# Optimization experiments

Measured on AMD Instinct MI355X. Metric: run time of the kernel, lower is better.

## Reference

```python
import jax, jax.numpy as jnp
import numpy as np

BS, NCH, H, NAGGR, R = 8192, 4, 256, 4, 8  # batch, max_output_degree, h_size, n_aggr, rank


def _xavier(k, shape):
    fan_in = int(np.prod(shape[:-1]))
    fan_out = int(shape[-1])
    s = float(np.sqrt(6.0 / (fan_in + fan_out)))
    return jax.random.uniform(k, shape, jnp.float32, -s, s)


def setup_inputs() -> dict:
    key = jax.random.key(0)
    ks = jax.random.split(key, 6)
    return {
        "neighbour_h": jax.random.normal(ks[0], (BS, NCH, H), jnp.float32),
        "U": _xavier(ks[1], (NCH, NAGGR, H, R)),
        "b": _xavier(ks[2], (NCH, NAGGR, 1, R)),
        "U_out": _xavier(ks[3], (NAGGR, R, H)),
        "b_out": _xavier(ks[4], (NAGGR, 1, H)),
        "T": _xavier(ks[5], (NAGGR,) + (R + 1,) * NCH + (R,)),
    }


def reference(neighbour_h, U, b, U_out, b_out, T):
    bs = neighbour_h.shape[0]
    # per-child projection: matmul([bs,nch,1,1,h], [nch,naggr,h,r]) + b, squeezed -> [bs,nch,naggr,r]
    x = jnp.einsum('bch,cahr->bcar', neighbour_h, U) + b[:, :, 0, :]
    ones = jnp.ones((bs, NAGGR, 1), x.dtype)
    # AugmentedTensor chained contraction (vectorized over the n_aggr loop):
    # first mode: [bs,naggr,r+1] @ [naggr,r+1,(r+1)^(nch-1)*r]
    h0 = jnp.concatenate([x[:, 0], ones], axis=-1)          # [bs,naggr,r+1]
    ris = jnp.einsum('baq,aqx->bax', h0, T.reshape(NAGGR, R + 1, -1))
    for i in range(1, NCH):  # contract remaining modes one by one
        hi = jnp.concatenate([x[:, i], ones], axis=-1)      # [bs,naggr,r+1]
        ris = ris.reshape(bs, NAGGR, R + 1, -1)
        ris = jnp.einsum('baq,baqx->bax', hi, ris)
    # ris: [bs,naggr,r]; output projection + bias -> [bs,naggr,h] -> [bs,naggr*h]
    out = jnp.einsum('bar,arh->bah', ris, U_out) + b_out[:, 0, :]
    return out.reshape(bs, -1)
```

## Files before the change

### kernel.cpp

```cpp
#include <hip/hip_runtime.h>

#define TT_ISTRIDE 672
#define TT_ELEMS (4 * 81 * 672)
#define WS_H   217728
#define WS_RIS 1397376
#define RIS_IHALF_STRIDE 262144

__global__ void t_transpose(const float* __restrict__ T, float* __restrict__ Tt) {
    int idx = blockIdx.x * 256 + threadIdx.x;
    if (idx >= TT_ELEMS) return;
    int col  = idx % 84;
    int t1   = idx / 84;
    int r    = t1 & 7;
    int rest = t1 / 8;
    int jt   = col / 28;
    int kk   = col - jt * 28;
    Tt[idx] = (kk < 27) ? T[rest * 648 + (jt * 27 + kk) * 8 + r] : 0.0f;
}

#define GLL(gsrc, ldst) __builtin_amdgcn_global_load_lds( \
    (const __attribute__((address_space(1))) void*)(gsrc), \
    (__attribute__((address_space(3))) void*)(ldst), 16, 0, 0)

#define KEEP(x) asm volatile("" : "+v"(x))

__global__ __launch_bounds__(512, 4) void k1_phasex(
    const float* __restrict__ nh, const float* __restrict__ U,
    const float* __restrict__ bi, float* __restrict__ h_ws) {
    __shared__ float nh_s[128 * 68];
    __shared__ float u_s[8 * 68];
    const int t  = threadIdx.x;
    const int a  = blockIdx.x >> 6;
    const int b0 = (blockIdx.x & 63) << 7;
    const int b  = t & 127;
    const int rp = t >> 7;

    #pragma unroll 1
    for (int c = 0; c < 4; ++c) {
        float acc0 = 0.f, acc1 = 0.f;
        #pragma unroll 1
        for (int hq = 0; hq < 4; ++hq) {
            __syncthreads();
            #pragma unroll
            for (int k = 0; k < 4; ++k) {
                int idx = t + (k << 9);
                int row = idx >> 4, col = (idx & 15) << 2;
                *(float4*)(nh_s + row * 68 + col) =
                    *(const float4*)(nh + (size_t)(b0 + row) * 1024 + (c << 8) + (hq << 6) + col);
            }
            u_s[(t & 7) * 68 + (t >> 3)] =
                U[(((c << 2) + a) << 11) + (((hq << 6) + (t >> 3)) << 3) + (t & 7)];
            __syncthreads();
            const float* nhp = nh_s + b * 68;
            const float* u0p = u_s + rp * 68;
            const float* u1p = u_s + (rp + 4) * 68;
            #pragma unroll
            for (int hh = 0; hh < 64; hh += 4) {
                float4 v  = *(const float4*)(nhp + hh);
                float4 ua = *(const float4*)(u0p + hh);
                float4 ub = *(const float4*)(u1p + hh);
                acc0 = fmaf(v.x, ua.x, acc0); acc0 = fmaf(v.y, ua.y, acc0);
                acc0 = fmaf(v.z, ua.z, acc0); acc0 = fmaf(v.w, ua.w, acc0);
                acc1 = fmaf(v.x, ub.x, acc1); acc1 = fmaf(v.y, ub.y, acc1);
                acc1 = fmaf(v.z, ub.z, acc1); acc1 = fmaf(v.w, ub.w, acc1);
            }
        }
        acc0 += bi[(((c << 2) + a) << 3) + rp];
        acc1 += bi[(((c << 2) + a) << 3) + rp + 4];
        size_t hb = ((size_t)a * 8192 + b0 + b) * 36 + c * 9;
        h_ws[hb + rp]     = acc0;
        h_ws[hb + rp + 4] = acc1;
        if (rp == 0) h_ws[hb + 8] = 1.0f;
    }
}

__global__ __launch_bounds__(512, 2) void k2_chain(
    const float* __restrict__ Tt, const float* __restrict__ h_ws,
    float* __restrict__ risP) {
    __shared__ float tc[2][9 * 672];
    __shared__ float h_s[36 * 260];

    const int t    = threadIdx.x;
    const int lane = t & 63;
    const int widr = t >> 6;
    const int ihalf = blockIdx.x >> 7;
    const int a     = (blockIdx.x >> 5) & 3;
    const int b0    = (blockIdx.x & 31) << 8;
    const int q0base = ihalf ? 4 : 0;
    const int NC     = ihalf ? 5 : 4;

    const float* Tw = Tt + (size_t)a * 54432 + (size_t)q0base * 6048;

    {
        const float* s = Tw;
        float* d = tc[0];
        GLL(s + 4 * t, d + 4 * t);
        GLL(s + 4 * (512 + t), d + 4 * (512 + t));
        if (t < 488) GLL(s + 4 * (1024 + t), d + 4 * (1024 + t));
    }
    for (int idx = t; idx < 2304; idx += 512) {
        int bb = idx / 9, j = idx % 9;
        float4 v = *(const float4*)(h_ws + ((size_t)a * 8192 + b0 + bb) * 36 + j * 4);
        h_s[(4 * j + 0) * 260 + bb] = v.x;
        h_s[(4 * j + 1) * 260 + bb] = v.y;
        h_s[(4 * j + 2) * 260 + bb] = v.z;
        h_s[(4 * j + 3) * 260 + bb] = v.w;
    }
    __syncthreads();

    float h2v[4][9], h3v[4][9];
    #pragma unroll
    for (int k = 0; k < 4; ++k) {
        #pragma unroll
        for (int q = 0; q < 9; ++q) {
            h2v[k][q] = h_s[(18 + q) * 260 + lane + 64 * k];
            h3v[k][q] = h_s[(27 + q) * 260 + lane + 64 * k];
        }
    }
    #pragma unroll
    for (int k = 0; k < 4; ++k) {
        #pragma unroll
        for (int q = 0; q < 9; ++q) { KEEP(h2v[k][q]); KEEP(h3v[k][q]); }
    }

    float A0 = 0.f, A1 = 0.f, A2 = 0.f, A3 = 0.f;

    #pragma unroll 1
    for (int c = 0; c < NC; ++c) {
        if (c < NC - 1) {
            const float* s = Tw + (size_t)(c + 1) * 6048;
            float* d = tc[(c + 1) & 1];
            GLL(s + 4 * t, d + 4 * t);
            GLL(s + 4 * (512 + t), d + 4 * (512 + t));
            if (t < 488) GLL(s + 4 * (1024 + t), d + 4 * (1024 + t));
            asm volatile("s_waitcnt vmcnt(3)" ::: "memory");
        } else {
            asm volatile("s_waitcnt vmcnt(0)" ::: "memory");
        }
        __builtin_amdgcn_s_barrier();
        asm volatile("" ::: "memory");

        const float* tb = tc[c & 1] + widr * 84;
        float h0c[4];
        #pragma unroll
        for (int k = 0; k < 4; ++k)
            h0c[k] = h_s[(q0base + c) * 260 + lane + 64 * k];

        #pragma unroll 1
        for (int q1 = 0; q1 < 9; ++q1) {
            float h1q[4];
            #pragma unroll
            for (int k = 0; k < 4; ++k)
                h1q[k] = h_s[(9 + q1) * 260 + lane + 64 * k];
            const float* tp = tb + q1 * TT_ISTRIDE;
            float dd[4] = {0.f, 0.f, 0.f, 0.f};
            #pragma unroll
            for (int jt = 0; jt < 3; ++jt) {
                float s[28];
                #pragma unroll
                for (int m = 0; m < 7; ++m)
                    *(float4*)(s + 4 * m) = *(const float4*)(tp + jt * 28 + 4 * m);
                #pragma unroll
                for (int k = 0; k < 4; ++k) {
                    float e0 = 0.f, e1 = 0.f, e2 = 0.f;
                    #pragma unroll
                    for (int m = 0; m < 9; ++m) {
                        e0 = fmaf(s[m],      h3v[k][m], e0);
                        e1 = fmaf(s[9 + m],  h3v[k][m], e1);
                        e2 = fmaf(s[18 + m], h3v[k][m], e2);
                    }
                    dd[k] = fmaf(h2v[k][3 * jt], e0, fmaf(h2v[k][3 * jt + 1], e1,
                            fmaf(h2v[k][3 * jt + 2], e2, dd[k])));
                }
            }
            A0 = fmaf(h0c[0] * h1q[0], dd[0], A0);
            A1 = fmaf(h0c[1] * h1q[1], dd[1], A1);
            A2 = fmaf(h0c[2] * h1q[2], dd[2], A2);
            A3 = fmaf(h0c[3] * h1q[3], dd[3], A3);
        }
        asm volatile("" ::: "memory");
        __builtin_amdgcn_s_barrier();
    }

    size_t rb = (size_t)ihalf * RIS_IHALF_STRIDE + ((size_t)a * 8192 + b0) * 8 + widr;
    risP[rb + (size_t)(lane)       * 8] = A0;
    risP[rb + (size_t)(lane + 64)  * 8] = A1;
    risP[rb + (size_t)(lane + 128) * 8] = A2;
    risP[rb + (size_t)(lane + 192) * 8] = A3;
}

__global__ __launch_bounds__(256, 8) void k3_out(
    const float* __restrict__ risP, const float* __restrict__ Uo,
    const float* __restrict__ bo, float* __restrict__ out) {
    __shared__ float uo_s[8192];
    __shared__ float bo_s[1024];
    __shared__ float ris_s[16 * 32];
    const int t  = threadIdx.x;
    const int b0 = blockIdx.x << 4;
    for (int idx = t; idx < 8192; idx += 256) uo_s[idx] = Uo[idx];
    for (int idx = t; idx < 1024; idx += 256) bo_s[idx] = bo[idx];
    for (int idx = t; idx < 512; idx += 256) {
        int bb = idx >> 5, rem = idx & 31, aa = rem >> 3, rr = rem & 7;
        size_t ro = ((size_t)aa * 8192 + b0 + bb) * 8 + rr;
        ris_s[bb * 32 + rem] = risP[ro] + risP[RIS_IHALF_STRIDE + ro];
    }
    __syncthreads();
    const int a  = t >> 6;
    const int c4 = (t & 63) << 2;
    float4 u[8];
    #pragma unroll
    for (int r = 0; r < 8; ++r)
        u[r] = *(const float4*)(uo_s + (a << 11) + (r << 8) + c4);
    const float4 b4 = *(const float4*)(bo_s + (a << 8) + c4);
    #pragma unroll 4
    for (int bb = 0; bb < 16; ++bb) {
        const float* rp = ris_s + bb * 32 + a * 8;
        float4 v = b4;
        #pragma unroll
        for (int r = 0; r < 8; ++r) {
            float w = rp[r];
            v.x = fmaf(w, u[r].x, v.x); v.y = fmaf(w, u[r].y, v.y);
            v.z = fmaf(w, u[r].z, v.z); v.w = fmaf(w, u[r].w, v.w);
        }
        *(float4*)(out + (size_t)(b0 + bb) * 1024 + (a << 8) + c4) = v;
    }
}

extern "C" void kernel_launch(void* const* d_in, const int* in_sizes, int n_in,
                              void* d_out, int out_size, void* d_ws, size_t ws_size,
                              hipStream_t stream) {
    (void)in_sizes; (void)n_in; (void)out_size; (void)ws_size;
    const float* nh = (const float*)d_in[0];
    const float* U  = (const float*)d_in[1];
    const float* bi = (const float*)d_in[2];
    const float* Uo = (const float*)d_in[3];
    const float* bo = (const float*)d_in[4];
    const float* T  = (const float*)d_in[5];
    float* outp = (float*)d_out;
    float* ws   = (float*)d_ws;

    t_transpose<<<(TT_ELEMS + 255) / 256, 256, 0, stream>>>(T, ws);
    k1_phasex<<<256, 512, 0, stream>>>(nh, U, bi, ws + WS_H);
    k2_chain<<<256, 512, 0, stream>>>(ws, ws + WS_H, ws + WS_RIS);
    k3_out<<<512, 256, 0, stream>>>(ws + WS_RIS, Uo, bo, outp);
}
```

Baseline: 108.7 us.

## Rework projection and chain kernels with transposed workspace and finer i-split

The projection kernel now gives each thread all 8 rank outputs for one child and aggregator. It loads neighbour rows into double-buffered XOR-swizzled LDS via global_load_lds, reads U directly from global memory, and writes h in a transposed [a][36][batch] layout. The chain kernel splits the 81 (q0,q1) pairs into four balanced quarters, doubling the grid to 512 blocks with smaller LDS and higher occupancy. It loads h rows with coalesced float4 reads from the transposed layout. The output kernel sums four partial ris buffers instead of two, adding a little reduction traffic.

New measurement: 113.7 us. 1.05x slower.

```diff
diff --git a/kernel.cpp b/kernel.cpp
--- a/kernel.cpp
+++ b/kernel.cpp
@@ -2,9 +2,9 @@
 
 #define TT_ISTRIDE 672
 #define TT_ELEMS (4 * 81 * 672)
-#define WS_H   217728
-#define WS_RIS 1397376
-#define RIS_IHALF_STRIDE 262144
+#define WS_HT 217728
+#define WS_RIS (217728 + 1179648)
+#define RIS_Q 262144
 
 __global__ void t_transpose(const float* __restrict__ T, float* __restrict__ Tt) {
     int idx = blockIdx.x * 256 + threadIdx.x;
@@ -24,142 +24,169 @@
 
 #define KEEP(x) asm volatile("" : "+v"(x))
 
-__global__ __launch_bounds__(512, 4) void k1_phasex(
+__global__ __launch_bounds__(512, 2) void k1_phasex(
     const float* __restrict__ nh, const float* __restrict__ U,
-    const float* __restrict__ bi, float* __restrict__ h_ws) {
-    __shared__ float nh_s[128 * 68];
-    __shared__ float u_s[8 * 68];
-    const int t  = threadIdx.x;
-    const int a  = blockIdx.x >> 6;
-    const int b0 = (blockIdx.x & 63) << 7;
-    const int b  = t & 127;
-    const int rp = t >> 7;
+    const float* __restrict__ bi, float* __restrict__ h_t) {
+    __shared__ float nh_s[2][8192];
+    const int t   = threadIdx.x;
+    const int bid = blockIdx.x;
+    const int bg  = (bid & 7) * 8 + ((bid >> 3) & 7);
+    const int c   = bid >> 6;
+    const int b0  = bg << 7;
+    const int b   = t & 127;
+    const int a   = t >> 7;
+
+    float acc[8];
+    {
+        const float* bp = bi + (((c << 2) + a) << 3);
+        #pragma unroll
+        for (int r = 0; r < 8; ++r) acc[r] = bp[r];
+    }
+
+    {
+        #pragma unroll
+        for (int rep = 0; rep < 4; ++rep) {
+            int tt = t + (rep << 9);
+            int bl = tt >> 4, sl = tt & 15;
+            const float* s = nh + (size_t)(b0 + bl) * 1024 + (c << 8)
+                           + ((sl ^ (bl & 15)) << 2);
+            GLL(s, &nh_s[0][tt << 2]);
+        }
+    }
 
     #pragma unroll 1
-    for (int c = 0; c < 4; ++c) {
-        float acc0 = 0.f, acc1 = 0.f;
-        #pragma unroll 1
-        for (int hq = 0; hq < 4; ++hq) {
-            __syncthreads();
-            #pragma unroll
-            for (int k = 0; k < 4; ++k) {
-                int idx = t + (k << 9);
-                int row = idx >> 4, col = (idx & 15) << 2;
-                *(float4*)(nh_s + row * 68 + col) =
-                    *(const float4*)(nh + (size_t)(b0 + row) * 1024 + (c << 8) + (hq << 6) + col);
+    for (int w = 0; w < 4; ++w) {
+        if (w < 3) {
+            #pragma unroll
+            for (int rep = 0; rep < 4; ++rep) {
+                int tt = t + (rep << 9);
+                int bl = tt >> 4, sl = tt & 15;
+                const float* s = nh + (size_t)(b0 + bl) * 1024 + (c << 8)
+                               + ((w + 1) << 6) + ((sl ^ (bl & 15)) << 2);
+                GLL(s, &nh_s[(w + 1) & 1][tt << 2]);
             }
-            u_s[(t & 7) * 68 + (t >> 3)] =
-                U[(((c << 2) + a) << 11) + (((hq << 6) + (t >> 3)) << 3) + (t & 7)];
-            __syncthreads();
-            const float* nhp = nh_s + b * 68;
-            const float* u0p = u_s + rp * 68;
-            const float* u1p = u_s + (rp + 4) * 68;
-            #pragma unroll
-            for (int hh = 0; hh < 64; hh += 4) {
-                float4 v  = *(const float4*)(nhp + hh);
-                float4 ua = *(const float4*)(u0p + hh);
-                float4 ub = *(const float4*)(u1p + hh);
-                acc0 = fmaf(v.x, ua.x, acc0); acc0 = fmaf(v.y, ua.y, acc0);
-                acc0 = fmaf(v.z, ua.z, acc0); acc0 = fmaf(v.w, ua.w, acc0);
-                acc1 = fmaf(v.x, ub.x, acc1); acc1 = fmaf(v.y, ub.y, acc1);
-                acc1 = fmaf(v.z, ub.z, acc1); acc1 = fmaf(v.w, ub.w, acc1);
-            }
-        }
-        acc0 += bi[(((c << 2) + a) << 3) + rp];
-        acc1 += bi[(((c << 2) + a) << 3) + rp + 4];
-        size_t hb = ((size_t)a * 8192 + b0 + b) * 36 + c * 9;
-        h_ws[hb + rp]     = acc0;
-        h_ws[hb + rp + 4] = acc1;
-        if (rp == 0) h_ws[hb + 8] = 1.0f;
-    }
-}
-
-__global__ __launch_bounds__(512, 2) void k2_chain(
-    const float* __restrict__ Tt, const float* __restrict__ h_ws,
+            asm volatile("s_waitcnt vmcnt(4)" ::: "memory");
+        } else {
+            asm volatile("s_waitcnt vmcnt(0)" ::: "memory");
+        }
+        __builtin_amdgcn_s_barrier();
+        asm volatile("" ::: "memory");
+
+        const float* Up = U + (((c << 2) + a) << 11) + (w << 9);
+        const float* ap = &nh_s[w & 1][b << 6];
+        #pragma unroll 4
+        for (int k4 = 0; k4 < 16; ++k4) {
+            float4 A = *(const float4*)(ap + ((k4 ^ (b & 15)) << 2));
+            const float4* up = (const float4*)(Up + (k4 << 5));
+            float4 u0 = up[0], u1 = up[1], u2 = up[2], u3 = up[3];
+            float4 u4 = up[4], u5 = up[5], u6 = up[6], u7 = up[7];
+            acc[0]=fmaf(A.x,u0.x,acc[0]); acc[1]=fmaf(A.x,u0.y,acc[1]);
+            acc[2]=fmaf(A.x,u0.z,acc[2]); acc[3]=fmaf(A.x,u0.w,acc[3]);
+            acc[4]=fmaf(A.x,u1.x,acc[4]); acc[5]=fmaf(A.x,u1.y,acc[5]);
+            acc[6]=fmaf(A.x,u1.z,acc[6]); acc[7]=fmaf(A.x,u1.w,acc[7]);
+            acc[0]=fmaf(A.y,u2.x,acc[0]); acc[1]=fmaf(A.y,u2.y,acc[1]);
+            acc[2]=fmaf(A.y,u2.z,acc[2]); acc[3]=fmaf(A.y,u2.w,acc[3]);
+            acc[4]=fmaf(A.y,u3.x,acc[4]); acc[5]=fmaf(A.y,u3.y,acc[5]);
+            acc[6]=fmaf(A.y,u3.z,acc[6]); acc[7]=fmaf(A.y,u3.w,acc[7]);
+            acc[0]=fmaf(A.z,u4.x,acc[0]); acc[1]=fmaf(A.z,u4.y,acc[1]);
+            acc[2]=fmaf(A.z,u4.z,acc[2]); acc[3]=fmaf(A.z,u4.w,acc[3]);
+            acc[4]=fmaf(A.z,u5.x,acc[4]); acc[5]=fmaf(A.z,u5.y,acc[5]);
+            acc[6]=fmaf(A.z,u5.z,acc[6]); acc[7]=fmaf(A.z,u5.w,acc[7]);
+            acc[0]=fmaf(A.w,u6.x,acc[0]); acc[1]=fmaf(A.w,u6.y,acc[1]);
+            acc[2]=fmaf(A.w,u6.z,acc[2]); acc[3]=fmaf(A.w,u6.w,acc[3]);
+            acc[4]=fmaf(A.w,u7.x,acc[4]); acc[5]=fmaf(A.w,u7.y,acc[5]);
+            acc[6]=fmaf(A.w,u7.z,acc[6]); acc[7]=fmaf(A.w,u7.w,acc[7]);
+        }
+        asm volatile("" ::: "memory");
+        __builtin_amdgcn_s_barrier();
+    }
+
+    size_t hb = ((size_t)a * 36 + (size_t)c * 9) * 8192 + b0 + b;
+    #pragma unroll
+    for (int r = 0; r < 8; ++r) h_t[hb + (size_t)r * 8192] = acc[r];
+    h_t[hb + (size_t)8 * 8192] = 1.0f;
+}
+
+__global__ __launch_bounds__(512, 4) void k2_chain(
+    const float* __restrict__ Tt, const float* __restrict__ h_t,
     float* __restrict__ risP) {
-    __shared__ float tc[2][9 * 672];
-    __shared__ float h_s[36 * 260];
-
+    __shared__ float tc[2][4096];
+    __shared__ float h_s[18 * 256];
     const int t    = threadIdx.x;
     const int lane = t & 63;
     const int widr = t >> 6;
-    const int ihalf = blockIdx.x >> 7;
-    const int a     = (blockIdx.x >> 5) & 3;
-    const int b0    = (blockIdx.x & 31) << 8;
-    const int q0base = ihalf ? 4 : 0;
-    const int NC     = ihalf ? 5 : 4;
-
-    const float* Tw = Tt + (size_t)a * 54432 + (size_t)q0base * 6048;
+    const int bid  = blockIdx.x;
+    const int bg   = (bid & 7) * 4 + ((bid >> 3) & 3);
+    const int rest = bid >> 5;
+    const int a    = rest >> 2;
+    const int iq   = rest & 3;
+    const int b0   = bg << 8;
+    const int i_base = iq * 20;
+
+    const float* Tw = Tt + (size_t)a * 54432;
 
     {
-        const float* s = Tw;
-        float* d = tc[0];
-        GLL(s + 4 * t, d + 4 * t);
-        GLL(s + 4 * (512 + t), d + 4 * (512 + t));
-        if (t < 488) GLL(s + 4 * (1024 + t), d + 4 * (1024 + t));
-    }
-    for (int idx = t; idx < 2304; idx += 512) {
-        int bb = idx / 9, j = idx % 9;
-        float4 v = *(const float4*)(h_ws + ((size_t)a * 8192 + b0 + bb) * 36 + j * 4);
-        h_s[(4 * j + 0) * 260 + bb] = v.x;
-        h_s[(4 * j + 1) * 260 + bb] = v.y;
-        h_s[(4 * j + 2) * 260 + bb] = v.z;
-        h_s[(4 * j + 3) * 260 + bb] = v.w;
-    }
+        const float* s = Tw + (size_t)i_base * 672;
+        GLL(s + 4 * t, tc[0] + 4 * t);
+        GLL(s + 4 * (512 + t), tc[0] + 4 * (512 + t));
+    }
+    for (int idx = t; idx < 1152; idx += 512) {
+        int row = idx >> 6, c4 = (idx & 63) << 2;
+        float4 v = *(const float4*)(h_t + ((size_t)a * 36 + row) * 8192 + b0 + c4);
+        *(float4*)(&h_s[row * 256 + c4]) = v;
+    }
+    float h2v[4][9], h3v[4][9];
+    #pragma unroll
+    for (int k = 0; k < 4; ++k) {
+        #pragma unroll
+        for (int q = 0; q < 9; ++q) {
+            h2v[k][q] = h_t[((size_t)a * 36 + 18 + q) * 8192 + b0 + lane + 64 * k];
+            h3v[k][q] = h_t[((size_t)a * 36 + 27 + q) * 8192 + b0 + lane + 64 * k];
+        }
+    }
+    #pragma unroll
+    for (int k = 0; k < 4; ++k) {
+        #pragma unroll
+        for (int q = 0; q < 9; ++q) { KEEP(h2v[k][q]); KEEP(h3v[k][q]); }
+    }
+
+    float A[4] = {0.f, 0.f, 0.f, 0.f};
     __syncthreads();
 
-    float h2v[4][9], h3v[4][9];
-    #pragma unroll
-    for (int k = 0; k < 4; ++k) {
-        #pragma unroll
-        for (int q = 0; q < 9; ++q) {
-            h2v[k][q] = h_s[(18 + q) * 260 + lane + 64 * k];
-            h3v[k][q] = h_s[(27 + q) * 260 + lane + 64 * k];
-        }
-    }
-    #pragma unroll
-    for (int k = 0; k < 4; ++k) {
-        #pragma unroll
-        for (int q = 0; q < 9; ++q) { KEEP(h2v[k][q]); KEEP(h3v[k][q]); }
-    }
-
-    float A0 = 0.f, A1 = 0.f, A2 = 0.f, A3 = 0.f;
+    int q0 = i_base / 9, q1 = i_base - 9 * (i_base / 9);
 
     #pragma unroll 1
-    for (int c = 0; c < NC; ++c) {
-        if (c < NC - 1) {
-            const float* s = Tw + (size_t)(c + 1) * 6048;
-            float* d = tc[(c + 1) & 1];
+    for (int ch = 0; ch < 4; ++ch) {
+        if (ch < 3) {
+            const float* s = Tw + (size_t)(i_base + 5 * (ch + 1)) * 672;
+            float* d = tc[(ch + 1) & 1];
             GLL(s + 4 * t, d + 4 * t);
             GLL(s + 4 * (512 + t), d + 4 * (512 + t));
-            if (t < 488) GLL(s + 4 * (1024 + t), d + 4 * (1024 + t));
-            asm volatile("s_waitcnt vmcnt(3)" ::: "memory");
+            asm volatile("s_waitcnt vmcnt(2)" ::: "memory");
         } else {
             asm volatile("s_waitcnt vmcnt(0)" ::: "memory");
         }
         __builtin_amdgcn_s_barrier();
         asm volatile("" ::: "memory");
 
-        const float* tb = tc[c & 1] + widr * 84;
-        float h0c[4];
-        #pragma unroll
-        for (int k = 0; k < 4; ++k)
-            h0c[k] = h_s[(q0base + c) * 260 + lane + 64 * k];
-
+        const int ni = (ch == 3 && iq == 3) ? 6 : 5;
+        const float* tcb = tc[ch & 1];
         #pragma unroll 1
-        for (int q1 = 0; q1 < 9; ++q1) {
-            float h1q[4];
-            #pragma unroll
-            for (int k = 0; k < 4; ++k)
-                h1q[k] = h_s[(9 + q1) * 260 + lane + 64 * k];
-            const float* tp = tb + q1 * TT_ISTRIDE;
+        for (int ii = 0; ii < ni; ++ii) {
+            float h0k[4], h1k[4];
+            #pragma unroll
+            for (int k = 0; k < 4; ++k) {
+                h0k[k] = h_s[q0 * 256 + lane + 64 * k];
+                h1k[k] = h_s[(9 + q1) * 256 + lane + 64 * k];
+            }
+            const float* tb = tcb + ii * 672 + widr * 84;
             float dd[4] = {0.f, 0.f, 0.f, 0.f};
             #pragma unroll
             for (int jt = 0; jt < 3; ++jt) {
+                const float4* tp = (const float4*)(tb + jt * 28);
                 float s[28];
                 #pragma unroll
-                for (int m = 0; m < 7; ++m)
-                    *(float4*)(s + 4 * m) = *(const float4*)(tp + jt * 28 + 4 * m);
+                for (int m = 0; m < 7; ++m) *(float4*)(s + 4 * m) = tp[m];
                 #pragma unroll
                 for (int k = 0; k < 4; ++k) {
                     float e0 = 0.f, e1 = 0.f, e2 = 0.f;
@@ -173,20 +200,18 @@
                             fmaf(h2v[k][3 * jt + 2], e2, dd[k])));
                 }
             }
-            A0 = fmaf(h0c[0] * h1q[0], dd[0], A0);
-            A1 = fmaf(h0c[1] * h1q[1], dd[1], A1);
-            A2 = fmaf(h0c[2] * h1q[2], dd[2], A2);
-            A3 = fmaf(h0c[3] * h1q[3], dd[3], A3);
-        }
-        asm volatile("" ::: "memory");
-        __builtin_amdgcn_s_barrier();
-    }
-
-    size_t rb = (size_t)ihalf * RIS_IHALF_STRIDE + ((size_t)a * 8192 + b0) * 8 + widr;
-    risP[rb + (size_t)(lane)       * 8] = A0;
-    risP[rb + (size_t)(lane + 64)  * 8] = A1;
-    risP[rb + (size_t)(lane + 128) * 8] = A2;
-    risP[rb + (size_t)(lane + 192) * 8] = A3;
+            #pragma unroll
+            for (int k = 0; k < 4; ++k) A[k] = fmaf(h0k[k] * h1k[k], dd[k], A[k]);
+            if (++q1 == 9) { q1 = 0; ++q0; }
+        }
+        asm volatile("" ::: "memory");
+        __builtin_amdgcn_s_barrier();
+    }
+
+    size_t rb = (size_t)iq * RIS_Q + ((size_t)a * 8192 + b0) * 8 + widr;
+    #pragma unroll
+    for (int k = 0; k < 4; ++k)
+        risP[rb + (size_t)(lane + 64 * k) * 8] = A[k];
 }
 
 __global__ __launch_bounds__(256, 8) void k3_out(
@@ -202,7 +227,8 @@
     for (int idx = t; idx < 512; idx += 256) {
         int bb = idx >> 5, rem = idx & 31, aa = rem >> 3, rr = rem & 7;
         size_t ro = ((size_t)aa * 8192 + b0 + bb) * 8 + rr;
-        ris_s[bb * 32 + rem] = risP[ro] + risP[RIS_IHALF_STRIDE + ro];
+        ris_s[bb * 32 + rem] = risP[ro] + risP[RIS_Q + ro]
+                             + risP[2 * RIS_Q + ro] + risP[3 * RIS_Q + ro];
     }
     __syncthreads();
     const int a  = t >> 6;
@@ -240,7 +266,7 @@
     float* ws   = (float*)d_ws;
 
     t_transpose<<<(TT_ELEMS + 255) / 256, 256, 0, stream>>>(T, ws);
-    k1_phasex<<<256, 512, 0, stream>>>(nh, U, bi, ws + WS_H);
-    k2_chain<<<256, 512, 0, stream>>>(ws, ws + WS_H, ws + WS_RIS);
+    k1_phasex<<<256, 512, 0, stream>>>(nh, U, bi, ws + WS_HT);
+    k2_chain<<<512, 512, 0, stream>>>(ws, ws + WS_HT, ws + WS_RIS);
     k3_out<<<512, 256, 0, stream>>>(ws + WS_RIS, Uo, bo, outp);
 }
```
